# Optimization experiments

Measured on AMD Instinct MI355X. Metric: run time of the kernel, lower is better.

The kernel has to match this reference:

```python
import jax, jax.numpy as jnp
import numpy as np

D_MODEL, N_HEADS, D_C, D_FF, N_EXPERTS, TOP_K = 1024, 16, 128, 2048, 8, 2
HEAD_DIM = D_MODEL // N_HEADS
THETA = 10000.0
RMS_EPS = float(np.finfo(np.float32).eps)  # torch nn.RMSNorm default eps


def rmsnorm(x, w):
    var = jnp.mean(x * x, axis=-1, keepdims=True)
    return x * jax.lax.rsqrt(var + RMS_EPS) * w


def rotate_half(x):
    x1, x2 = jnp.split(x, 2, axis=-1)
    return jnp.concatenate([-x2, x1], axis=-1)


def rope_cos_sin(ts):
    # ts: (B, L) float timestamps -> cos, sin: (B, L, HEAD_DIM)
    freqs = 1.0 / THETA ** (jnp.arange(0, HEAD_DIM, 2, dtype=jnp.float32) / HEAD_DIM)
    t = ts[..., None] * freqs            # (B, L, HEAD_DIM//2)
    emb = jnp.concatenate([t, t], axis=-1)
    return jnp.cos(emb), jnp.sin(emb)


def setup_inputs() -> dict:
    key = jax.random.key(0)
    ks = jax.random.split(key, 16)
    B, L, D = 4, 1024, D_MODEL
    s = 0.02
    inp = {
        "x": jax.random.normal(ks[0], (B, L, D), jnp.float32),
        "timestamps_q": jnp.tile(jnp.arange(L, dtype=jnp.float32), (B, 1)),
        "timestamps_kv": jnp.tile(jnp.arange(L, dtype=jnp.float32), (B, 1)),
        "attn_norm_w": jnp.ones((D,), jnp.float32),
        "ffn_norm_w": jnp.ones((D,), jnp.float32),
        "w_kv_c": jax.random.normal(ks[1], (D_C, D), jnp.float32) * s,
        "w_kc_up": jax.random.normal(ks[2], (D, D_C), jnp.float32) * s,
        "w_vc_up": jax.random.normal(ks[3], (D, D_C), jnp.float32) * s,
        "w_qr": jax.random.normal(ks[4], (D, D), jnp.float32) * s,
        "w_kr": jax.random.normal(ks[5], (D, D), jnp.float32) * s,
        "w_o": jax.random.normal(ks[6], (D, D), jnp.float32) * s,
        "gate_w": jax.random.normal(ks[7], (N_EXPERTS, D), jnp.float32) * s,
        "expert_bias": jnp.zeros((N_EXPERTS,), jnp.float32),
        "w1": jax.random.normal(ks[8], (N_EXPERTS, 2 * D_FF, D), jnp.float32) * s,
        "w2": jax.random.normal(ks[9], (N_EXPERTS, D, 2 * D_FF), jnp.float32) * s,
    }
    return inp


def reference(x, timestamps_q, timestamps_kv, attn_norm_w, ffn_norm_w,
              w_kv_c, w_kc_up, w_vc_up, w_qr, w_kr, w_o,
              gate_w, expert_bias, w1, w2):
    B, L, D = x.shape
    H, hd = N_HEADS, HEAD_DIM
    scale = hd ** -0.5

    # ---- MLA attention (pre-norm) ----
    h = rmsnorm(x, attn_norm_w)
    c_kv = h @ w_kv_c.T                                    # (B,L,d_c)
    k_c = (c_kv @ w_kc_up.T).reshape(B, L, H, hd).transpose(0, 2, 1, 3)
    v_c = (c_kv @ w_vc_up.T).reshape(B, L, H, hd).transpose(0, 2, 1, 3)
    q_r = (h @ w_qr.T).reshape(B, L, H, hd).transpose(0, 2, 1, 3)
    k_r = (h @ w_kr.T).reshape(B, L, H, hd).transpose(0, 2, 1, 3)

    cos_q, _sin_q = rope_cos_sin(timestamps_q)
    cos_k, _sin_k = rope_cos_sin(timestamps_kv)
    cos_q = cos_q[:, None]  # (B,1,L,hd)
    cos_k = cos_k[:, None]
    # Faithful to source: apply_rotary_pos_emb(q, k, cos_q, cos_k) -> sin := cos_k
    q_r = q_r * cos_q + rotate_half(q_r) * cos_k
    k_r = k_r * cos_q + rotate_half(k_r) * cos_k

    qs = q_r * scale
    attn = jnp.einsum("bhqd,bhkd->bhqk", qs, k_c) + jnp.einsum("bhqd,bhkd->bhqk", qs, k_r)
    attn_w = jax.nn.softmax(attn, axis=-1)
    out = jnp.einsum("bhqk,bhkd->bhqd", attn_w, v_c)
    out = out.transpose(0, 2, 1, 3).reshape(B, L, D) @ w_o.T
    x1 = x + out

    # ---- MoE FFN (pre-norm) ----
    hn = rmsnorm(x1, ffn_norm_w).reshape(-1, D)            # (T, D)
    T = hn.shape[0]
    gate_logits = hn @ gate_w.T + expert_bias              # (T, E)
    gate_probs = jax.nn.softmax(gate_logits, axis=-1)
    topk_w, topk_i = jax.lax.top_k(gate_probs, TOP_K)
    topk_w = topk_w / jnp.sum(topk_w, axis=-1, keepdims=True)

    # dense (T, E) routing weights (top-k indices are unique per token)
    wd = jnp.zeros((T, N_EXPERTS), x.dtype).at[jnp.arange(T)[:, None], topk_i].add(topk_w)

    hmid = jax.nn.silu(jnp.einsum("td,ekd->tek", hn, w1))  # (T,E,2*d_ff)
    y = jnp.einsum("tek,edk->ted", hmid, w2)               # (T,E,D)
    moe_out = jnp.einsum("ted,te->td", y, wd).reshape(B, L, D)

    expert_counts = jnp.zeros((N_EXPERTS,), jnp.float32).at[topk_i.ravel()].add(1.0)
    return x1 + moe_out, expert_counts
```

## Files before the change

kernel.cpp:

```cpp
#include <hip/hip_runtime.h>
#include <hip/hip_bf16.h>

typedef __hip_bfloat16 bf16;
typedef __attribute__((ext_vector_type(8))) unsigned short ushort8v;
typedef __bf16 bf16x8 __attribute__((ext_vector_type(8)));
typedef float f32x4 __attribute__((ext_vector_type(4)));

#define NTOK 4096
#define DMODEL 1024
#define NHEADS 16
#define HD 64
#define DC 128
#define DFF2 4096
#define NEXP 8
#define LSEQ 1024
#define NBATCH 4
#define RMS_EPS 1.1920928955078125e-07f

union U8 { ushort8v u; bf16x8 b; };

__device__ __forceinline__ float bf2f(unsigned short u) {
  return __uint_as_float(((unsigned int)u) << 16);
}
__device__ __forceinline__ unsigned short f2bf(float f) {
  unsigned int u = __float_as_uint(f);
  unsigned int r = (u + 0x7FFF + ((u >> 16) & 1)) >> 16;
  return (unsigned short)r;
}
__device__ __forceinline__ void gload_lds16(const unsigned short* g, unsigned short* l) {
  __builtin_amdgcn_global_load_lds(
      (__attribute__((address_space(1))) void*)(const_cast<unsigned short*>(g)),
      (__attribute__((address_space(3))) void*)(l), 16, 0, 0);
}

__global__ __launch_bounds__(256)
void rmsnorm_kernel(const float* __restrict__ x, const float* __restrict__ w,
                    float* __restrict__ o, unsigned short* __restrict__ ob) {
  int t = blockIdx.x;
  int tid = threadIdx.x;
  const float4* xr = (const float4*)(x + (size_t)t * DMODEL);
  float4 v = xr[tid];
  float ss = v.x * v.x + v.y * v.y + v.z * v.z + v.w * v.w;
#pragma unroll
  for (int off = 32; off > 0; off >>= 1) ss += __shfl_xor(ss, off);
  __shared__ float red[4];
  int wid = tid >> 6, lane = tid & 63;
  if (lane == 0) red[wid] = ss;
  __syncthreads();
  float tot = red[0] + red[1] + red[2] + red[3];
  float scale = rsqrtf(tot * (1.0f / DMODEL) + RMS_EPS);
  float4 wv = ((const float4*)w)[tid];
  float4 ov;
  ov.x = v.x * scale * wv.x;
  ov.y = v.y * scale * wv.y;
  ov.z = v.z * scale * wv.z;
  ov.w = v.w * scale * wv.w;
  if (o) ((float4*)(o + (size_t)t * DMODEL))[tid] = ov;
  if (ob) {
    unsigned short* orow = ob + (size_t)t * DMODEL + tid * 4;
    orow[0] = f2bf(ov.x); orow[1] = f2bf(ov.y);
    orow[2] = f2bf(ov.z); orow[3] = f2bf(ov.w);
  }
}

__global__ __launch_bounds__(256)
void cvt_bf16_kernel(const float* __restrict__ in, unsigned short* __restrict__ o, int n8) {
  int stride = gridDim.x * 256;
  for (int i = blockIdx.x * 256 + threadIdx.x; i < n8; i += stride) {
    float4 a = ((const float4*)in)[2 * i];
    float4 b = ((const float4*)in)[2 * i + 1];
    ushort8v u;
    u[0] = f2bf(a.x); u[1] = f2bf(a.y); u[2] = f2bf(a.z); u[3] = f2bf(a.w);
    u[4] = f2bf(b.x); u[5] = f2bf(b.y); u[6] = f2bf(b.z); u[7] = f2bf(b.w);
    *(ushort8v*)(o + (size_t)i * 8) = u;
  }
}

__global__ __launch_bounds__(256)
void cvt3_bf16_kernel(const float* __restrict__ s0, int n0,
                      const float* __restrict__ s1, int n1,
                      const float* __restrict__ s2, int n2,
                      unsigned short* __restrict__ o) {
  int total = n0 + n1 + n2;
  int stride = gridDim.x * 256;
  for (int i = blockIdx.x * 256 + threadIdx.x; i < total; i += stride) {
    const float* src;
    int li = i;
    if (li < n0) src = s0;
    else if ((li -= n0) < n1) src = s1;
    else { li -= n1; src = s2; }
    float4 a = ((const float4*)src)[2 * li];
    float4 b = ((const float4*)src)[2 * li + 1];
    ushort8v u;
    u[0] = f2bf(a.x); u[1] = f2bf(a.y); u[2] = f2bf(a.z); u[3] = f2bf(a.w);
    u[4] = f2bf(b.x); u[5] = f2bf(b.y); u[6] = f2bf(b.z); u[7] = f2bf(b.w);
    *(ushort8v*)(o + (size_t)i * 8) = u;
  }
}

__global__ __launch_bounds__(256)
void gemm_bf16(const unsigned short* __restrict__ Ab, const unsigned short* __restrict__ Wb,
               float* __restrict__ Cf, const float* __restrict__ addend, int N, int K) {
  __shared__ __align__(16) unsigned short As[128 * 64];
  __shared__ __align__(16) unsigned short Bs[128 * 64];
  int row0 = blockIdx.y * 128;
  int col0 = blockIdx.x * 128;
  int tid = threadIdx.x;
  int w = tid >> 6, l = tid & 63;
  int lr = l >> 3;
  int lc = (l & 7) * 8;

  const unsigned short* aSrc[4];
  const unsigned short* bSrc[4];
#pragma unroll
  for (int i = 0; i < 4; ++i) {
    aSrc[i] = Ab + (size_t)(row0 + i * 32 + w * 8 + lr) * K + lc;
    bSrc[i] = Wb + (size_t)(col0 + i * 32 + w * 8 + lr) * K + lc;
  }

  f32x4 acc[4][4] = {};
  int wr = w >> 1, wc = w & 1;
  int ln = l & 15, lq = l >> 4;

  for (int k0 = 0; k0 < K; k0 += 64) {
#pragma unroll
    for (int i = 0; i < 4; ++i) {
      gload_lds16(aSrc[i] + k0, &As[(i * 4 + w) * 512]);
      gload_lds16(bSrc[i] + k0, &Bs[(i * 4 + w) * 512]);
    }
    __syncthreads();
#pragma unroll
    for (int kk = 0; kk < 2; ++kk) {
      bf16x8 af[4], bfr[4];
#pragma unroll
      for (int m = 0; m < 4; ++m)
        af[m] = *(const bf16x8*)&As[(wr * 64 + m * 16 + ln) * 64 + kk * 32 + lq * 8];
#pragma unroll
      for (int n = 0; n < 4; ++n)
        bfr[n] = *(const bf16x8*)&Bs[(wc * 64 + n * 16 + ln) * 64 + kk * 32 + lq * 8];
#pragma unroll
      for (int m = 0; m < 4; ++m)
#pragma unroll
        for (int n = 0; n < 4; ++n)
          acc[m][n] = __builtin_amdgcn_mfma_f32_16x16x32_bf16(af[m], bfr[n], acc[m][n], 0, 0, 0);
    }
    __syncthreads();
  }

#pragma unroll
  for (int m = 0; m < 4; ++m) {
#pragma unroll
    for (int j = 0; j < 4; ++j) {
      int row = row0 + wr * 64 + m * 16 + lq * 4 + j;
      float* crow = Cf + (size_t)row * N + col0 + wc * 64 + ln;
      const float* arow = addend ? addend + (size_t)row * N + col0 + wc * 64 + ln : nullptr;
#pragma unroll
      for (int n = 0; n < 4; ++n) {
        float vv = acc[m][n][j];
        if (addend) vv += arow[n * 16];
        crow[n * 16] = vv;
      }
    }
  }
}

__global__ __launch_bounds__(256)
void gemm_proj(const unsigned short* __restrict__ Ab, const unsigned short* __restrict__ Wcat,
               float* __restrict__ d0, float* __restrict__ d1, float* __restrict__ d2,
               unsigned short* __restrict__ d1b,
               int c1, int c2, int s0, int s1, int s2, int K) {
  __shared__ __align__(16) unsigned short As[128 * 64];
  __shared__ __align__(16) unsigned short Bs[128 * 64];
  int row0 = blockIdx.y * 128;
  int col0 = blockIdx.x * 128;
  int tid = threadIdx.x;
  int w = tid >> 6, l = tid & 63;
  int lr = l >> 3;
  int lc = (l & 7) * 8;

  const unsigned short* aSrc[4];
  const unsigned short* bSrc[4];
#pragma unroll
  for (int i = 0; i < 4; ++i) {
    aSrc[i] = Ab + (size_t)(row0 + i * 32 + w * 8 + lr) * K + lc;
    bSrc[i] = Wcat + (size_t)(col0 + i * 32 + w * 8 + lr) * K + lc;
  }

  f32x4 acc[4][4] = {};
  int wr = w >> 1, wc = w & 1;
  int ln = l & 15, lq = l >> 4;

  for (int k0 = 0; k0 < K; k0 += 64) {
#pragma unroll
    for (int i = 0; i < 4; ++i) {
      gload_lds16(aSrc[i] + k0, &As[(i * 4 + w) * 512]);
      gload_lds16(bSrc[i] + k0, &Bs[(i * 4 + w) * 512]);
    }
    __syncthreads();
#pragma unroll
    for (int kk = 0; kk < 2; ++kk) {
      bf16x8 af[4], bfr[4];
#pragma unroll
      for (int m = 0; m < 4; ++m)
        af[m] = *(const bf16x8*)&As[(wr * 64 + m * 16 + ln) * 64 + kk * 32 + lq * 8];
#pragma unroll
      for (int n = 0; n < 4; ++n)
        bfr[n] = *(const bf16x8*)&Bs[(wc * 64 + n * 16 + ln) * 64 + kk * 32 + lq * 8];
#pragma unroll
      for (int m = 0; m < 4; ++m)
#pragma unroll
        for (int n = 0; n < 4; ++n)
          acc[m][n] = __builtin_amdgcn_mfma_f32_16x16x32_bf16(af[m], bfr[n], acc[m][n], 0, 0, 0);
    }
    __syncthreads();
  }

  bool seg1 = (col0 >= c1) && (col0 < c2);
  if (seg1 && d1b) {
#pragma unroll
    for (int m = 0; m < 4; ++m) {
#pragma unroll
      for (int j = 0; j < 4; ++j) {
        int row = row0 + wr * 64 + m * 16 + lq * 4 + j;
        unsigned short* crow = d1b + (size_t)row * s1 + (col0 - c1) + wc * 64 + ln;
#pragma unroll
        for (int n = 0; n < 4; ++n) crow[n * 16] = f2bf(acc[m][n][j]);
      }
    }
    return;
  }
  float* dst;
  int cb, stride;
  if (col0 < c1) { dst = d0; cb = 0; stride = s0; }
  else if (seg1) { dst = d1; cb = c1; stride = s1; }
  else { dst = d2; cb = c2; stride = s2; }
#pragma unroll
  for (int m = 0; m < 4; ++m) {
#pragma unroll
    for (int j = 0; j < 4; ++j) {
      int row = row0 + wr * 64 + m * 16 + lq * 4 + j;
      float* crow = dst + (size_t)row * stride + (col0 - cb) + wc * 64 + ln;
#pragma unroll
      for (int n = 0; n < 4; ++n) crow[n * 16] = acc[m][n][j];
    }
  }
}

template <int MODE>
__global__ __launch_bounds__(256)
void moe_mfma(const unsigned short* __restrict__ A, const unsigned short* __restrict__ Wb,
              unsigned short* __restrict__ Cout, const int* __restrict__ tok2e,
              const int* __restrict__ ebase, const int* __restrict__ icnt) {
  constexpr int N = (MODE == 0) ? DFF2 : DMODEL;
  constexpr int K = (MODE == 0) ? DMODEL : DFF2;
  __shared__ __align__(16) unsigned short As[128 * 64];
  __shared__ __align__(16) unsigned short Bs[128 * 64];
  int e = blockIdx.z;
  int base = ebase[e];
  int cnt = icnt[e];
  int row0 = blockIdx.y * 128;
  if (row0 >= cnt) return;
  int col0 = blockIdx.x * 128;
  int tid = threadIdx.x;
  int w = tid >> 6, l = tid & 63;
  int lr = l >> 3;
  int lc = (l & 7) * 8;

  const unsigned short* aSrc[4];
  const unsigned short* bSrc[4];
#pragma unroll
  for (int i = 0; i < 4; ++i) {
    int r = row0 + i * 32 + w * 8 + lr;
    r = r < cnt ? r : cnt - 1;
    if (MODE == 0) {
      int tok = tok2e[base + r] >> 1;
      aSrc[i] = A + (size_t)tok * K + lc;
    } else {
      aSrc[i] = A + (size_t)(base + r) * K + lc;
    }
    int nrow = col0 + i * 32 + w * 8 + lr;
    bSrc[i] = Wb + (size_t)e * N * K + (size_t)nrow * K + lc;
  }

  f32x4 acc[4][4] = {};
  int wr = w >> 1, wc = w & 1;
  int ln16 = l & 15, lq = l >> 4;

  for (int k0 = 0; k0 < K; k0 += 64) {
#pragma unroll
    for (int i = 0; i < 4; ++i) {
      gload_lds16(aSrc[i] + k0, &As[(i * 4 + w) * 512]);
      gload_lds16(bSrc[i] + k0, &Bs[(i * 4 + w) * 512]);
    }
    __syncthreads();
#pragma unroll
    for (int kk = 0; kk < 2; ++kk) {
      bf16x8 af[4], bfr[4];
#pragma unroll
      for (int m = 0; m < 4; ++m)
        af[m] = *(const bf16x8*)&As[(wr * 64 + m * 16 + ln16) * 64 + kk * 32 + lq * 8];
#pragma unroll
      for (int n = 0; n < 4; ++n)
        bfr[n] = *(const bf16x8*)&Bs[(wc * 64 + n * 16 + ln16) * 64 + kk * 32 + lq * 8];
#pragma unroll
      for (int m = 0; m < 4; ++m)
#pragma unroll
        for (int n = 0; n < 4; ++n)
          acc[m][n] = __builtin_amdgcn_mfma_f32_16x16x32_bf16(af[m], bfr[n], acc[m][n], 0, 0, 0);
    }
    __syncthreads();
  }

#pragma unroll
  for (int m = 0; m < 4; ++m) {
#pragma unroll
    for (int j = 0; j < 4; ++j) {
      int r = row0 + wr * 64 + m * 16 + lq * 4 + j;
      if (r < cnt) {
        if (MODE == 0) {
          unsigned short* orow = Cout + (size_t)(base + r) * N + col0 + wc * 64 + ln16;
#pragma unroll
          for (int n = 0; n < 4; ++n) {
            float v = acc[m][n][j];
            float s = v / (1.f + __expf(-v));
            orow[n * 16] = f2bf(s);
          }
        } else {
          int t2 = tok2e[base + r];
          unsigned short* orow = Cout + (size_t)t2 * N + col0 + wc * 64 + ln16;
#pragma unroll
          for (int n = 0; n < 4; ++n) orow[n * 16] = f2bf(acc[m][n][j]);
        }
      }
    }
  }
}

__global__ __launch_bounds__(256)
void rope_qk_kernel(const float* __restrict__ q, const float* __restrict__ k,
                    const float* __restrict__ kc, const float* __restrict__ tsq,
                    const float* __restrict__ tskv,
                    unsigned short* __restrict__ Qb, unsigned short* __restrict__ Kb) {
  int t = blockIdx.x;
  int tid = threadIdx.x;
  __shared__ float cq[32], ck[32];
  if (tid < 32) {
    float fr = __expf(-(float)(2 * tid) * (1.0f / HD) * 9.210340371976184f);
    cq[tid] = cosf(tsq[t] * fr);
    ck[tid] = cosf(tskv[t] * fr);
  }
  __syncthreads();
  int b = t >> 10, lrow = t & 1023;
  size_t rb = (size_t)t * DMODEL;
  for (int p = tid; p < 512; p += 256) {
    int hh = p >> 5, d = p & 31;
    int c1 = hh * 64 + d, c2 = c1 + 32;
    float cqd = cq[d], ckd = ck[d];
    float q1 = q[rb + c1], q2 = q[rb + c2];
    float rq1 = (q1 * cqd - q2 * ckd) * 0.125f;
    float rq2 = (q2 * cqd + q1 * ckd) * 0.125f;
    float k1 = k[rb + c1], k2 = k[rb + c2];
    float rk1 = (k1 * cqd - k2 * ckd) + kc[rb + c1];
    float rk2 = (k2 * cqd + k1 * ckd) + kc[rb + c2];
    size_t dst = ((size_t)(b * NHEADS + hh) * LSEQ + lrow) * HD;
    Qb[dst + d] = f2bf(rq1);
    Qb[dst + d + 32] = f2bf(rq2);
    Kb[dst + d] = f2bf(rk1);
    Kb[dst + d + 32] = f2bf(rk2);
  }
}

__global__ __launch_bounds__(256)
void v_split_kernel(const unsigned short* __restrict__ vbb, unsigned short* __restrict__ Vt) {
  __shared__ unsigned short tile[128][72];
  int bh = blockIdx.x;
  int lt = blockIdx.y;
  int b = bh >> 4, hh = bh & 15;
  int tid = threadIdx.x;
#pragma unroll
  for (int pass = 0; pass < 8; ++pass) {
    int r = pass * 16 + (tid >> 4);
    int dq = (tid & 15) * 4;
    ushort4 vv = *(const ushort4*)(vbb + (size_t)(b * 1024 + lt * 128 + r) * DMODEL + hh * 64 + dq);
    tile[r][dq + 0] = vv.x; tile[r][dq + 1] = vv.y;
    tile[r][dq + 2] = vv.z; tile[r][dq + 3] = vv.w;
  }
  __syncthreads();
  int d = tid >> 2, seg = (tid & 3) * 32;
  size_t obase = ((size_t)bh * HD + d) * LSEQ + lt * 128 + seg;
  for (int i = 0; i < 32; i += 4) {
    ushort4 u;
    u.x = tile[seg + i][d];
    u.y = tile[seg + i + 1][d];
    u.z = tile[seg + i + 2][d];
    u.w = tile[seg + i + 3][d];
    *(ushort4*)(Vt + obase + i) = u;
  }
}

__global__ __launch_bounds__(256, 2)
void attn_mfma(const unsigned short* __restrict__ Qb, const unsigned short* __restrict__ Kb,
               const unsigned short* __restrict__ Vt, unsigned short* __restrict__ ao) {
  __shared__ unsigned int plds[128 * 128];
  int bh = blockIdx.y;
  int qt = blockIdx.x;
  int tid = threadIdx.x;
  int w = tid >> 6, l = tid & 63;
  int ln = l & 15, lq = l >> 4;
  size_t kvbase = (size_t)bh * LSEQ * HD;
  int qrow0 = qt * 128 + w * 32;

  bf16x8 qh[2][2];
#pragma unroll
  for (int mi = 0; mi < 2; ++mi)
#pragma unroll
    for (int ks = 0; ks < 2; ++ks) {
      size_t o = kvbase + (size_t)(qrow0 + mi * 16 + ln) * HD + ks * 32 + lq * 8;
      qh[mi][ks] = *(const bf16x8*)(Qb + o);
    }

  float l_run[2][4] = {};
  f32x4 oacc[2][4] = {};

  for (int kt = 0; kt < 8; ++kt) {
    int k0 = kt * 128;
    f32x4 sacc[2][8] = {};
#pragma unroll
    for (int ni = 0; ni < 8; ++ni) {
      size_t ko = kvbase + (size_t)(k0 + ni * 16 + ln) * HD + lq * 8;
      bf16x8 kh0 = *(const bf16x8*)(Kb + ko);
      bf16x8 kh1 = *(const bf16x8*)(Kb + ko + 32);
#pragma unroll
      for (int mi = 0; mi < 2; ++mi) {
        f32x4 a = sacc[mi][ni];
        a = __builtin_amdgcn_mfma_f32_16x16x32_bf16(qh[mi][0], kh0, a, 0, 0, 0);
        a = __builtin_amdgcn_mfma_f32_16x16x32_bf16(qh[mi][1], kh1, a, 0, 0, 0);
        sacc[mi][ni] = a;
      }
    }
#pragma unroll
    for (int mi = 0; mi < 2; ++mi)
#pragma unroll
      for (int j = 0; j < 4; ++j) {
        float rs = 0.f;
#pragma unroll
        for (int ni = 0; ni < 8; ++ni) {
          float p = __expf(sacc[mi][ni][j]);
          sacc[mi][ni][j] = p;
          rs += p;
        }
        rs += __shfl_xor(rs, 1);
        rs += __shfl_xor(rs, 2);
        rs += __shfl_xor(rs, 4);
        rs += __shfl_xor(rs, 8);
        l_run[mi][j] += rs;
      }
#pragma unroll
    for (int mi = 0; mi < 2; ++mi)
#pragma unroll
      for (int ni = 0; ni < 8; ++ni)
#pragma unroll
        for (int j = 0; j < 4; ++j) {
          int row = w * 32 + mi * 16 + lq * 4 + j;
          int col = ni * 16 + ln;
          unsigned int u = ((unsigned int)f2bf(sacc[mi][ni][j])) << 16;
          plds[row * 128 + (col ^ ((row & 3) << 3))] = u;
        }
    __syncthreads();
#pragma unroll
    for (int ksp = 0; ksp < 4; ++ksp) {
      bf16x8 ph[2];
#pragma unroll
      for (int mi = 0; mi < 2; ++mi) {
        int row = w * 32 + mi * 16 + ln;
        int c0 = ksp * 32 + lq * 8;
        const unsigned int* pp = &plds[row * 128 + (c0 ^ ((row & 3) << 3))];
        uint4 u0 = *(const uint4*)pp;
        uint4 u1 = *(const uint4*)(pp + 4);
        unsigned int uu[8] = {u0.x, u0.y, u0.z, u0.w, u1.x, u1.y, u1.z, u1.w};
        U8 uh;
#pragma unroll
        for (int jj = 0; jj < 8; ++jj) uh.u[jj] = (unsigned short)(uu[jj] >> 16);
        ph[mi] = uh.b;
      }
#pragma unroll
      for (int ni = 0; ni < 4; ++ni) {
        size_t vo = kvbase + (size_t)(ni * 16 + ln) * LSEQ + k0 + ksp * 32 + lq * 8;
        bf16x8 vh = *(const bf16x8*)(Vt + vo);
#pragma unroll
        for (int mi = 0; mi < 2; ++mi)
          oacc[mi][ni] = __builtin_amdgcn_mfma_f32_16x16x32_bf16(ph[mi], vh, oacc[mi][ni], 0, 0, 0);
      }
    }
    __syncthreads();
  }

  int b = bh >> 4, hh = bh & 15;
#pragma unroll
  for (int mi = 0; mi < 2; ++mi) {
    float inv[4];
#pragma unroll
    for (int j = 0; j < 4; ++j) inv[j] = 1.0f / l_run[mi][j];
#pragma unroll
    for (int ni = 0; ni < 4; ++ni)
#pragma unroll
      for (int j = 0; j < 4; ++j) {
        int tok = b * 1024 + qt * 128 + w * 32 + mi * 16 + lq * 4 + j;
        int col = hh * 64 + ni * 16 + ln;
        ao[(size_t)tok * DMODEL + col] = f2bf(oacc[mi][ni][j] * inv[j]);
      }
  }
}

__global__ __launch_bounds__(256)
void gate_kernel(const float* __restrict__ hn, const float* __restrict__ gw,
                 const float* __restrict__ bias, int* __restrict__ ti,
                 float* __restrict__ tw, int* __restrict__ icnt,
                 float* __restrict__ counts_out) {
  int t = blockIdx.x * 4 + (threadIdx.x >> 6);
  int lane = threadIdx.x & 63;
  const float* hrow = hn + (size_t)t * DMODEL;
  float acc[NEXP];
#pragma unroll
  for (int e = 0; e < NEXP; ++e) acc[e] = 0.f;
  for (int d = lane; d < DMODEL; d += 64) {
    float hv = hrow[d];
#pragma unroll
    for (int e = 0; e < NEXP; ++e) acc[e] += hv * gw[e * DMODEL + d];
  }
#pragma unroll
  for (int e = 0; e < NEXP; ++e)
#pragma unroll
    for (int off = 32; off > 0; off >>= 1) acc[e] += __shfl_xor(acc[e], off);
  if (lane == 0) {
    float lg[NEXP], ex[NEXP];
    float mx = -1e30f;
#pragma unroll
    for (int e = 0; e < NEXP; ++e) {
      lg[e] = acc[e] + bias[e];
      mx = fmaxf(mx, lg[e]);
    }
#pragma unroll
    for (int e = 0; e < NEXP; ++e) ex[e] = expf(lg[e] - mx);
    int i0 = 0;
    float p0 = ex[0];
#pragma unroll
    for (int e = 1; e < NEXP; ++e)
      if (ex[e] > p0) { p0 = ex[e]; i0 = e; }
    int i1 = -1;
    float p1 = -1.f;
#pragma unroll
    for (int e = 0; e < NEXP; ++e)
      if (e != i0 && ex[e] > p1) { p1 = ex[e]; i1 = e; }
    float wsum = p0 + p1;
    ti[2 * t] = i0;
    ti[2 * t + 1] = i1;
    tw[2 * t] = p0 / wsum;
    tw[2 * t + 1] = p1 / wsum;
    atomicAdd(&icnt[i0], 1);
    atomicAdd(&icnt[i1], 1);
    atomicAdd(&counts_out[i0], 1.0f);
    atomicAdd(&counts_out[i1], 1.0f);
  }
}

__global__ void init_kernel(float* __restrict__ counts_out, int* __restrict__ icnt,
                            int* __restrict__ cursor) {
  int i = threadIdx.x;
  if (i < NEXP) {
    counts_out[i] = 0.f;
    icnt[i] = 0;
    cursor[i] = 0;
  }
}

__global__ void scan_kernel(const int* __restrict__ icnt, int* __restrict__ ebase) {
  if (threadIdx.x == 0) {
    int s = 0;
    for (int e = 0; e < NEXP; ++e) {
      ebase[e] = s;
      s += icnt[e];
    }
  }
}

__global__ __launch_bounds__(256)
void scatter_kernel(const int* __restrict__ ti, const int* __restrict__ ebase,
                    int* __restrict__ cursor, int* __restrict__ tok2e) {
  int t = blockIdx.x * 256 + threadIdx.x;
#pragma unroll
  for (int s = 0; s < 2; ++s) {
    int e = ti[2 * t + s];
    int pos = atomicAdd(&cursor[e], 1);
    tok2e[ebase[e] + pos] = 2 * t + s;
  }
}

__global__ __launch_bounds__(256)
void combine_kernel(const float* __restrict__ x1, const unsigned short* __restrict__ y,
                    const float* __restrict__ tw, float* __restrict__ out) {
  int idx = blockIdx.x * 256 + threadIdx.x;
  int t = idx >> 8, c = idx & 255;
  float w0 = tw[2 * t], w1 = tw[2 * t + 1];
  float4 a = ((const float4*)x1)[idx];
  const unsigned short* y0 = y + (size_t)(2 * t) * DMODEL + c * 4;
  const unsigned short* y1 = y0 + DMODEL;
  ushort4 u0 = *(const ushort4*)y0;
  ushort4 u1 = *(const ushort4*)y1;
  float4 o;
  o.x = a.x + w0 * bf2f(u0.x) + w1 * bf2f(u1.x);
  o.y = a.y + w0 * bf2f(u0.y) + w1 * bf2f(u1.y);
  o.z = a.z + w0 * bf2f(u0.z) + w1 * bf2f(u1.z);
  o.w = a.w + w0 * bf2f(u0.w) + w1 * bf2f(u1.w);
  ((float4*)out)[idx] = o;
}

extern "C" void kernel_launch(void* const* d_in, const int* in_sizes, int n_in,
                              void* d_out, int out_size, void* d_ws, size_t ws_size,
                              hipStream_t stream) {
  (void)in_sizes; (void)n_in; (void)ws_size;
  const float* x = (const float*)d_in[0];
  const float* tsq = (const float*)d_in[1];
  const float* tskv = (const float*)d_in[2];
  const float* attn_nw = (const float*)d_in[3];
  const float* ffn_nw = (const float*)d_in[4];
  const float* w_kv_c = (const float*)d_in[5];
  const float* w_kc_up = (const float*)d_in[6];
  const float* w_vc_up = (const float*)d_in[7];
  const float* w_qr = (const float*)d_in[8];
  const float* w_kr = (const float*)d_in[9];
  const float* w_o = (const float*)d_in[10];
  const float* gate_w = (const float*)d_in[11];
  const float* expert_bias = (const float*)d_in[12];
  const float* w1 = (const float*)d_in[13];
  const float* w2 = (const float*)d_in[14];

  float* out = (float*)d_out;
  float* counts_out = out + (out_size - NEXP);

  char* ws = (char*)d_ws;
  size_t off = 0;
  auto alloc = [&](size_t bytes) {
    char* p = ws + off;
    off += (bytes + 255) & ~(size_t)255;
    return p;
  };
  float* h   = (float*)alloc((size_t)NTOK * DMODEL * 4);
  float* qb  = (float*)alloc((size_t)NTOK * DMODEL * 4);
  float* kb  = (float*)alloc((size_t)NTOK * DMODEL * 4);
  float* vb  = (float*)alloc((size_t)NTOK * DMODEL * 4);
  float* kcb = (float*)alloc((size_t)NTOK * DMODEL * 4);
  float* ckv = (float*)alloc((size_t)NTOK * DC * 4);
  unsigned short* yb  = (unsigned short*)alloc((size_t)NTOK * 2 * DMODEL * 2);
  unsigned short* hb  = (unsigned short*)alloc((size_t)NTOK * DMODEL * 2);
  unsigned short* hmid = (unsigned short*)alloc((size_t)NTOK * 2 * DFF2 * 2);
  unsigned short* ckvb = (unsigned short*)alloc((size_t)NTOK * DC * 2);
  unsigned short* wbuf = (unsigned short*)alloc((size_t)2176 * DMODEL * 2);
  float* tw  = (float*)alloc((size_t)NTOK * 2 * 4);
  int* ti    = (int*)alloc((size_t)NTOK * 2 * 4);
  int* tok2e = (int*)alloc((size_t)NTOK * 2 * 4);
  int* icnt  = (int*)alloc(NEXP * 4);
  int* ebase = (int*)alloc(NEXP * 4);
  int* cursor = (int*)alloc(NEXP * 4);

  unsigned short* vbb = (unsigned short*)vb;
  unsigned short* Qb = hmid;
  unsigned short* Kb = hmid + (size_t)4 * 1024 * 1024;
  unsigned short* Vt = hmid + (size_t)8 * 1024 * 1024;
  unsigned short* ao = hmid + (size_t)12 * 1024 * 1024;
  unsigned short* wxb = (unsigned short*)qb;

  init_kernel<<<1, 64, 0, stream>>>(counts_out, icnt, cursor);
  rmsnorm_kernel<<<NTOK, 256, 0, stream>>>(x, attn_nw, nullptr, hb);
  cvt3_bf16_kernel<<<1024, 256, 0, stream>>>(w_qr, DMODEL * DMODEL / 8,
                                             w_kr, DMODEL * DMODEL / 8,
                                             w_kv_c, DC * DMODEL / 8, wbuf);
  gemm_proj<<<dim3(17, 32), 256, 0, stream>>>(hb, wbuf, qb, kb, ckv, nullptr,
                                              1024, 2048, DMODEL, DMODEL, DC, DMODEL);
  cvt_bf16_kernel<<<256, 256, 0, stream>>>(ckv, ckvb, NTOK * DC / 8);
  cvt3_bf16_kernel<<<64, 256, 0, stream>>>(w_kc_up, DMODEL * DC / 8,
                                           w_vc_up, DMODEL * DC / 8,
                                           w_vc_up, 0, wbuf);
  gemm_proj<<<dim3(16, 32), 256, 0, stream>>>(ckvb, wbuf, kcb, nullptr, nullptr, vbb,
                                              1024, 2048, DMODEL, DMODEL, DMODEL, DC);
  rope_qk_kernel<<<NTOK, 256, 0, stream>>>(qb, kb, kcb, tsq, tskv, Qb, Kb);
  v_split_kernel<<<dim3(64, 8), 256, 0, stream>>>(vbb, Vt);
  attn_mfma<<<dim3(8, 64), 256, 0, stream>>>(Qb, Kb, Vt, ao);
  cvt_bf16_kernel<<<512, 256, 0, stream>>>(w_o, wbuf, DMODEL * DMODEL / 8);
  gemm_bf16<<<dim3(8, 32), 256, 0, stream>>>(ao, wbuf, h, x, DMODEL, DMODEL);
  rmsnorm_kernel<<<NTOK, 256, 0, stream>>>(h, ffn_nw, qb, hb);
  gate_kernel<<<NTOK / 4, 256, 0, stream>>>(qb, gate_w, expert_bias, ti, tw, icnt, counts_out);
  scan_kernel<<<1, 64, 0, stream>>>(icnt, ebase);
  scatter_kernel<<<NTOK / 256, 256, 0, stream>>>(ti, ebase, cursor, tok2e);
  cvt_bf16_kernel<<<2048, 256, 0, stream>>>(w1, wxb, NEXP * DFF2 * DMODEL / 8);
  moe_mfma<0><<<dim3(DFF2 / 128, NTOK / 128, NEXP), 256, 0, stream>>>(hb, wxb, hmid, tok2e, ebase, icnt);
  cvt_bf16_kernel<<<2048, 256, 0, stream>>>(w2, wxb, NEXP * DMODEL * DFF2 / 8);
  moe_mfma<1><<<dim3(DMODEL / 128, NTOK / 128, NEXP), 256, 0, stream>>>(hmid, wxb, yb, tok2e, ebase, icnt);
  combine_kernel<<<NTOK, 256, 0, stream>>>(h, yb, tw, out);
}
```

Before: 763.9 us.

## Run MoE expert GEMMs in FP8 with scaled weights and FP8 activations

Switches both MoE expert GEMMs from bf16 to FP8 (e4m3) MFMA. Weights are scaled by a constant before quantization, the FFN RMSNorm output and the SiLU intermediate are written as FP8, and accumulators are rescaled on output. This halves memory traffic and LDS footprint for the dominant FFN work and uses the higher-rate FP8 matrix instructions. The risk is accuracy loss from FP8 quantization with a fixed scale, and the LDS access pattern now uses 8-byte fragment loads.

```diff
diff --git a/kernel.cpp b/kernel.cpp
--- a/kernel.cpp
+++ b/kernel.cpp
@@ -16,6 +16,8 @@
 #define LSEQ 1024
 #define NBATCH 4
 #define RMS_EPS 1.1920928955078125e-07f
+#define WSCALE 32.0f
+#define WISCALE 0.03125f
 
 union U8 { ushort8v u; bf16x8 b; };
 
@@ -27,15 +29,38 @@
   unsigned int r = (u + 0x7FFF + ((u >> 16) & 1)) >> 16;
   return (unsigned short)r;
 }
+__device__ __forceinline__ unsigned char f2fp8(float f) {
+  unsigned int u = __float_as_uint(f);
+  unsigned int s = (u >> 24) & 0x80u;
+  float a = fabsf(f);
+  if (!(a < 448.f)) a = 448.f;
+  if (a < 0.015625f) {
+    int m = (int)rintf(a * 512.f);
+    return (unsigned char)(s | (unsigned)m);
+  }
+  unsigned int b = __float_as_uint(a);
+  b += 0x000FFFFFu + ((b >> 20) & 1u);
+  int e = (int)((b >> 23) & 0xFF) - 127;
+  if (e > 8) return (unsigned char)(s | 0x7E);
+  unsigned int code = s | ((unsigned int)(e + 7) << 3) | ((b >> 20) & 7u);
+  if ((code & 0x7F) > 0x7E) code = s | 0x7E;
+  return (unsigned char)code;
+}
 __device__ __forceinline__ void gload_lds16(const unsigned short* g, unsigned short* l) {
   __builtin_amdgcn_global_load_lds(
       (__attribute__((address_space(1))) void*)(const_cast<unsigned short*>(g)),
       (__attribute__((address_space(3))) void*)(l), 16, 0, 0);
 }
+__device__ __forceinline__ void gload_lds16b(const unsigned char* g, unsigned char* l) {
+  __builtin_amdgcn_global_load_lds(
+      (__attribute__((address_space(1))) void*)(const_cast<unsigned char*>(g)),
+      (__attribute__((address_space(3))) void*)(l), 16, 0, 0);
+}
 
 __global__ __launch_bounds__(256)
 void rmsnorm_kernel(const float* __restrict__ x, const float* __restrict__ w,
-                    float* __restrict__ o, unsigned short* __restrict__ ob) {
+                    float* __restrict__ o, unsigned short* __restrict__ ob,
+                    unsigned char* __restrict__ o8) {
   int t = blockIdx.x;
   int tid = threadIdx.x;
   const float4* xr = (const float4*)(x + (size_t)t * DMODEL);
@@ -61,6 +86,12 @@
     orow[0] = f2bf(ov.x); orow[1] = f2bf(ov.y);
     orow[2] = f2bf(ov.z); orow[3] = f2bf(ov.w);
   }
+  if (o8) {
+    uchar4 q;
+    q.x = f2fp8(ov.x); q.y = f2fp8(ov.y);
+    q.z = f2fp8(ov.z); q.w = f2fp8(ov.w);
+    *(uchar4*)(o8 + (size_t)t * DMODEL + tid * 4) = q;
+  }
 }
 
 __global__ __launch_bounds__(256)
@@ -73,6 +104,21 @@
     u[0] = f2bf(a.x); u[1] = f2bf(a.y); u[2] = f2bf(a.z); u[3] = f2bf(a.w);
     u[4] = f2bf(b.x); u[5] = f2bf(b.y); u[6] = f2bf(b.z); u[7] = f2bf(b.w);
     *(ushort8v*)(o + (size_t)i * 8) = u;
+  }
+}
+
+__global__ __launch_bounds__(256)
+void cvt_fp8_kernel(const float* __restrict__ in, unsigned char* __restrict__ o, int n8) {
+  int stride = gridDim.x * 256;
+  for (int i = blockIdx.x * 256 + threadIdx.x; i < n8; i += stride) {
+    float4 a = ((const float4*)in)[2 * i];
+    float4 b = ((const float4*)in)[2 * i + 1];
+    unsigned char q[8];
+    q[0] = f2fp8(WSCALE * a.x); q[1] = f2fp8(WSCALE * a.y);
+    q[2] = f2fp8(WSCALE * a.z); q[3] = f2fp8(WSCALE * a.w);
+    q[4] = f2fp8(WSCALE * b.x); q[5] = f2fp8(WSCALE * b.y);
+    q[6] = f2fp8(WSCALE * b.z); q[7] = f2fp8(WSCALE * b.w);
+    *(unsigned long*)(o + (size_t)i * 8) = *(const unsigned long*)q;
   }
 }
 
@@ -248,13 +294,14 @@
 
 template <int MODE>
 __global__ __launch_bounds__(256)
-void moe_mfma(const unsigned short* __restrict__ A, const unsigned short* __restrict__ Wb,
-              unsigned short* __restrict__ Cout, const int* __restrict__ tok2e,
-              const int* __restrict__ ebase, const int* __restrict__ icnt) {
+void moe_fp8(const unsigned char* __restrict__ A, const unsigned char* __restrict__ W8,
+             unsigned char* __restrict__ C8, unsigned short* __restrict__ Cb,
+             const int* __restrict__ tok2e, const int* __restrict__ ebase,
+             const int* __restrict__ icnt) {
   constexpr int N = (MODE == 0) ? DFF2 : DMODEL;
   constexpr int K = (MODE == 0) ? DMODEL : DFF2;
-  __shared__ __align__(16) unsigned short As[128 * 64];
-  __shared__ __align__(16) unsigned short Bs[128 * 64];
+  __shared__ __align__(16) unsigned char As[128 * 64];
+  __shared__ __align__(16) unsigned char Bs[128 * 64];
   int e = blockIdx.z;
   int base = ebase[e];
   int cnt = icnt[e];
@@ -263,14 +310,14 @@
   int col0 = blockIdx.x * 128;
   int tid = threadIdx.x;
   int w = tid >> 6, l = tid & 63;
-  int lr = l >> 3;
-  int lc = (l & 7) * 8;
-
-  const unsigned short* aSrc[4];
-  const unsigned short* bSrc[4];
-#pragma unroll
-  for (int i = 0; i < 4; ++i) {
-    int r = row0 + i * 32 + w * 8 + lr;
+  int lr = l >> 2;
+  int lc = (l & 3) * 16;
+
+  const unsigned char* aSrc[2];
+  const unsigned char* bSrc[2];
+#pragma unroll
+  for (int i = 0; i < 2; ++i) {
+    int r = row0 + i * 64 + w * 16 + lr;
     r = r < cnt ? r : cnt - 1;
     if (MODE == 0) {
       int tok = tok2e[base + r] >> 1;
@@ -278,35 +325,35 @@
     } else {
       aSrc[i] = A + (size_t)(base + r) * K + lc;
     }
-    int nrow = col0 + i * 32 + w * 8 + lr;
-    bSrc[i] = Wb + (size_t)e * N * K + (size_t)nrow * K + lc;
+    int nrow = col0 + i * 64 + w * 16 + lr;
+    bSrc[i] = W8 + (size_t)e * N * K + (size_t)nrow * K + lc;
   }
 
   f32x4 acc[4][4] = {};
   int wr = w >> 1, wc = w & 1;
-  int ln16 = l & 15, lq = l >> 4;
+  int ln = l & 15, lq = l >> 4;
 
   for (int k0 = 0; k0 < K; k0 += 64) {
 #pragma unroll
-    for (int i = 0; i < 4; ++i) {
-      gload_lds16(aSrc[i] + k0, &As[(i * 4 + w) * 512]);
-      gload_lds16(bSrc[i] + k0, &Bs[(i * 4 + w) * 512]);
+    for (int i = 0; i < 2; ++i) {
+      gload_lds16b(aSrc[i] + k0, &As[(i * 64 + w * 16) * 64]);
+      gload_lds16b(bSrc[i] + k0, &Bs[(i * 64 + w * 16) * 64]);
     }
     __syncthreads();
 #pragma unroll
     for (int kk = 0; kk < 2; ++kk) {
-      bf16x8 af[4], bfr[4];
+      long af[4], bfr[4];
 #pragma unroll
       for (int m = 0; m < 4; ++m)
-        af[m] = *(const bf16x8*)&As[(wr * 64 + m * 16 + ln16) * 64 + kk * 32 + lq * 8];
+        af[m] = *(const long*)&As[(wr * 64 + m * 16 + ln) * 64 + kk * 32 + lq * 8];
 #pragma unroll
       for (int n = 0; n < 4; ++n)
-        bfr[n] = *(const bf16x8*)&Bs[(wc * 64 + n * 16 + ln16) * 64 + kk * 32 + lq * 8];
+        bfr[n] = *(const long*)&Bs[(wc * 64 + n * 16 + ln) * 64 + kk * 32 + lq * 8];
 #pragma unroll
       for (int m = 0; m < 4; ++m)
 #pragma unroll
         for (int n = 0; n < 4; ++n)
-          acc[m][n] = __builtin_amdgcn_mfma_f32_16x16x32_bf16(af[m], bfr[n], acc[m][n], 0, 0, 0);
+          acc[m][n] = __builtin_amdgcn_mfma_f32_16x16x32_fp8_fp8(af[m], bfr[n], acc[m][n], 0, 0, 0);
     }
     __syncthreads();
   }
@@ -318,18 +365,18 @@
       int r = row0 + wr * 64 + m * 16 + lq * 4 + j;
       if (r < cnt) {
         if (MODE == 0) {
-          unsigned short* orow = Cout + (size_t)(base + r) * N + col0 + wc * 64 + ln16;
+          unsigned char* orow = C8 + (size_t)(base + r) * N + col0 + wc * 64 + ln;
 #pragma unroll
           for (int n = 0; n < 4; ++n) {
-            float v = acc[m][n][j];
+            float v = acc[m][n][j] * WISCALE;
             float s = v / (1.f + __expf(-v));
-            orow[n * 16] = f2bf(s);
+            orow[n * 16] = f2fp8(s);
           }
         } else {
           int t2 = tok2e[base + r];
-          unsigned short* orow = Cout + (size_t)t2 * N + col0 + wc * 64 + ln16;
-#pragma unroll
-          for (int n = 0; n < 4; ++n) orow[n * 16] = f2bf(acc[m][n][j]);
+          unsigned short* orow = Cb + (size_t)t2 * N + col0 + wc * 64 + ln;
+#pragma unroll
+          for (int n = 0; n < 4; ++n) orow[n * 16] = f2bf(acc[m][n][j] * WISCALE);
         }
       }
     }
@@ -662,16 +709,18 @@
   int* icnt  = (int*)alloc(NEXP * 4);
   int* ebase = (int*)alloc(NEXP * 4);
   int* cursor = (int*)alloc(NEXP * 4);
+  unsigned char* hn8 = (unsigned char*)alloc((size_t)NTOK * DMODEL);
 
   unsigned short* vbb = (unsigned short*)vb;
   unsigned short* Qb = hmid;
   unsigned short* Kb = hmid + (size_t)4 * 1024 * 1024;
   unsigned short* Vt = hmid + (size_t)8 * 1024 * 1024;
   unsigned short* ao = hmid + (size_t)12 * 1024 * 1024;
-  unsigned short* wxb = (unsigned short*)qb;
+  unsigned char* hmid8 = (unsigned char*)(hmid + (size_t)16 * 1024 * 1024);
+  unsigned char* wx8 = (unsigned char*)qb;
 
   init_kernel<<<1, 64, 0, stream>>>(counts_out, icnt, cursor);
-  rmsnorm_kernel<<<NTOK, 256, 0, stream>>>(x, attn_nw, nullptr, hb);
+  rmsnorm_kernel<<<NTOK, 256, 0, stream>>>(x, attn_nw, nullptr, hb, nullptr);
   cvt3_bf16_kernel<<<1024, 256, 0, stream>>>(w_qr, DMODEL * DMODEL / 8,
                                              w_kr, DMODEL * DMODEL / 8,
                                              w_kv_c, DC * DMODEL / 8, wbuf);
@@ -688,13 +737,15 @@
   attn_mfma<<<dim3(8, 64), 256, 0, stream>>>(Qb, Kb, Vt, ao);
   cvt_bf16_kernel<<<512, 256, 0, stream>>>(w_o, wbuf, DMODEL * DMODEL / 8);
   gemm_bf16<<<dim3(8, 32), 256, 0, stream>>>(ao, wbuf, h, x, DMODEL, DMODEL);
-  rmsnorm_kernel<<<NTOK, 256, 0, stream>>>(h, ffn_nw, qb, hb);
+  rmsnorm_kernel<<<NTOK, 256, 0, stream>>>(h, ffn_nw, qb, nullptr, hn8);
   gate_kernel<<<NTOK / 4, 256, 0, stream>>>(qb, gate_w, expert_bias, ti, tw, icnt, counts_out);
   scan_kernel<<<1, 64, 0, stream>>>(icnt, ebase);
   scatter_kernel<<<NTOK / 256, 256, 0, stream>>>(ti, ebase, cursor, tok2e);
-  cvt_bf16_kernel<<<2048, 256, 0, stream>>>(w1, wxb, NEXP * DFF2 * DMODEL / 8);
-  moe_mfma<0><<<dim3(DFF2 / 128, NTOK / 128, NEXP), 256, 0, stream>>>(hb, wxb, hmid, tok2e, ebase, icnt);
-  cvt_bf16_kernel<<<2048, 256, 0, stream>>>(w2, wxb, NEXP * DMODEL * DFF2 / 8);
-  moe_mfma<1><<<dim3(DMODEL / 128, NTOK / 128, NEXP), 256, 0, stream>>>(hmid, wxb, yb, tok2e, ebase, icnt);
+  cvt_fp8_kernel<<<2048, 256, 0, stream>>>(w1, wx8, NEXP * DFF2 * DMODEL / 8);
+  moe_fp8<0><<<dim3(DFF2 / 128, NTOK / 128, NEXP), 256, 0, stream>>>(
+      hn8, wx8, hmid8, nullptr, tok2e, ebase, icnt);
+  cvt_fp8_kernel<<<2048, 256, 0, stream>>>(w2, wx8, NEXP * DMODEL * DFF2 / 8);
+  moe_fp8<1><<<dim3(DMODEL / 128, NTOK / 128, NEXP), 256, 0, stream>>>(
+      hmid8, wx8, nullptr, yb, tok2e, ebase, icnt);
   combine_kernel<<<NTOK, 256, 0, stream>>>(h, yb, tw, out);
 }
```

Result: slower. 856.0 us (+12.1%).
